# Kernel tuning notes

Measured on AMD Instinct MI355X. Metric: run time of the kernel, lower is better.

Reference implementation:

```python
import jax, jax.numpy as jnp
import numpy as np

B, S, E, H = 2, 2048, 1024, 16
HD = E // H
DFF = 4 * E
LN_EPS = 1e-5


def _layernorm(x, g, b):
    mu = jnp.mean(x, axis=-1, keepdims=True)
    var = jnp.mean(jnp.square(x - mu), axis=-1, keepdims=True)
    return (x - mu) * jax.lax.rsqrt(var + LN_EPS) * g + b


def setup_inputs() -> dict:
    key = jax.random.key(0)
    ks = jax.random.split(key, 6)
    inp = {
        "x": jax.random.normal(ks[0], (B, S, E), jnp.float32),
        "ln1_g": jnp.ones((E,), jnp.float32),
        "ln1_b": jnp.zeros((E,), jnp.float32),
        "ln2_g": jnp.ones((E,), jnp.float32),
        "ln2_b": jnp.zeros((E,), jnp.float32),
        # OptimizedPoincareBallLinear init: randn * 0.1, zero bias
        "w_qkv": jax.random.normal(ks[1], (3 * E, E), jnp.float32) * 0.1,
        "b_qkv": jnp.zeros((3 * E,), jnp.float32),
        "w_ao": jax.random.normal(ks[2], (E, E), jnp.float32) * 0.1,
        "b_ao": jnp.zeros((E,), jnp.float32),
        "w_fc": jax.random.normal(ks[3], (DFF, E), jnp.float32) * 0.1,
        "b_fc": jnp.zeros((DFF,), jnp.float32),
        "w_po": jax.random.normal(ks[4], (E, DFF), jnp.float32) * 0.1,
        "b_po": jnp.zeros((E,), jnp.float32),
    }
    return inp


def reference(x, ln1_g, ln1_b, ln2_g, ln2_b, w_qkv, b_qkv, w_ao, b_ao,
              w_fc, b_fc, w_po, b_po):
    # --- attention branch ---
    h = _layernorm(x, ln1_g, ln1_b)
    qkv = h @ w_qkv.T + b_qkv                       # [B,S,3E]
    qkv = qkv.reshape(B, S, H, 3 * HD).transpose(0, 2, 1, 3)  # [B,H,S,3hd]
    q, k, v = jnp.split(qkv, 3, axis=-1)            # each [B,H,S,hd]
    scores = jnp.einsum('bhqd,bhkd->bhqk', q, k) / jnp.sqrt(
        jnp.asarray(HD, jnp.float32))
    causal = jnp.tril(jnp.ones((S, S), bool))        # attn_bias[:, :, :S, :S]
    scores = jnp.where(causal, scores, jnp.finfo(scores.dtype).min)
    attn_w = jax.nn.softmax(scores, axis=-1)         # dropout p=0.1 inactive (eval)
    attn = jnp.einsum('bhqk,bhkd->bhqd', attn_w, v)  # [B,H,S,hd]
    attn = attn.transpose(0, 2, 1, 3).reshape(B, S, E)
    attn = attn @ w_ao.T + b_ao
    x = x + attn
    # --- MLP branch ---
    h2 = _layernorm(x, ln2_g, ln2_b)
    h2 = h2 @ w_fc.T + b_fc
    h2 = jax.nn.gelu(h2, approximate=True)           # GPT-2 gelu_new
    h2 = h2 @ w_po.T + b_po
    x = x + h2
    return x
```

## Files before the change

kernel.cpp:

```cpp
#include <hip/hip_runtime.h>
#include <cstddef>
#include <cstdint>

#define Bc 2
#define Sc 2048
#define Ec 1024
#define Hc 16
#define HDc 64
#define DFFc 4096
#define ROWS (Bc * Sc)

typedef _Float16 half8v __attribute__((ext_vector_type(8)));
typedef _Float16 half4v __attribute__((ext_vector_type(4)));
typedef float f32x4 __attribute__((ext_vector_type(4)));
typedef _Float16 h16;

__device__ inline void gld_lds16(const void* g, void* l) {
    __builtin_amdgcn_global_load_lds(
        (const __attribute__((address_space(1))) void*)g,
        (__attribute__((address_space(3))) void*)l, 16, 0, 0);
}

__device__ inline float gelu_new(float x) {
    float x2 = x * x;
    float u = x * fmaf(0.07135481627362f, x2, 1.5957691216057308f);
    return x / (1.0f + __expf(-u));
}

__global__ __launch_bounds__(256) void cvt4_kernel(
    const float* __restrict__ a,
    const float* __restrict__ b,
    const float* __restrict__ c,
    const float* __restrict__ d,
    h16* __restrict__ out)
{
    int bid = blockIdx.x;
    const float* src;
    size_t obase;
    int base;
    if (bid < 3072)      { src = a; obase = 0;       base = bid; }
    else if (bid < 4096) { src = b; obase = 3145728; base = bid - 3072; }
    else if (bid < 8192) { src = c; obase = 4194304; base = bid - 4096; }
    else                 { src = d; obase = 8388608; base = bid - 8192; }
    int i = base * 1024 + threadIdx.x * 4;
    float4 v = *(const float4*)(src + i);
    half4v o;
    o.x = (h16)v.x; o.y = (h16)v.y; o.z = (h16)v.z; o.w = (h16)v.w;
    *(half4v*)(out + obase + i) = o;
}

__device__ inline float block_sum256(float v, float* sb) {
    #pragma unroll
    for (int o = 32; o > 0; o >>= 1) v += __shfl_down(v, o, 64);
    int lane = threadIdx.x & 63, w = threadIdx.x >> 6;
    if (lane == 0) sb[w] = v;
    __syncthreads();
    float r = sb[0] + sb[1] + sb[2] + sb[3];
    __syncthreads();
    return r;
}

__global__ __launch_bounds__(256) void ln_kernel(const float* __restrict__ x,
                                                 const float* __restrict__ g,
                                                 const float* __restrict__ b,
                                                 h16* __restrict__ out) {
    __shared__ float sb[4];
    int row = blockIdx.x;
    int t = threadIdx.x;
    const float* xr = x + (size_t)row * Ec;
    float4 v = ((const float4*)xr)[t];
    float s = v.x + v.y + v.z + v.w;
    float mu = block_sum256(s, sb) * (1.0f / Ec);
    float dx = v.x - mu, dy = v.y - mu, dz = v.z - mu, dw = v.w - mu;
    float ss = dx * dx + dy * dy + dz * dz + dw * dw;
    float var = block_sum256(ss, sb) * (1.0f / Ec);
    float inv = rsqrtf(var + 1e-5f);
    float4 gv = ((const float4*)g)[t];
    float4 bv = ((const float4*)b)[t];
    half4v o;
    o.x = (h16)(dx * inv * gv.x + bv.x);
    o.y = (h16)(dy * inv * gv.y + bv.y);
    o.z = (h16)(dz * inv * gv.z + bv.z);
    o.w = (h16)(dw * inv * gv.w + bv.w);
    ((half4v*)(out + (size_t)row * Ec))[t] = o;
}

template <int EPI, typename OutT>
__global__ __launch_bounds__(256) void gemm_mfma(
    const h16* __restrict__ A, const h16* __restrict__ W,
    const float* __restrict__ bias, const float* __restrict__ R,
    OutT* __restrict__ C, int M, int N, int K)
{
    __shared__ h16 As[2][128 * 32];
    __shared__ h16 Ws[2][128 * 32];

    const int t = threadIdx.x;
    const int lane = t & 63, wv = t >> 6;
    const int wm = wv >> 1, wn = wv & 1;
    const int c15 = lane & 15, q = lane >> 4;
    const int row0 = blockIdx.y * 128, col0 = blockIdx.x * 128;
    const int arow = t >> 2, acol = (t & 3) << 3;

    const h16* ap0 = A + (size_t)(row0 + arow) * K + acol;
    const h16* ap1 = ap0 + (size_t)64 * K;
    const h16* wp0 = W + (size_t)(col0 + arow) * K + acol;
    const h16* wp1 = wp0 + (size_t)64 * K;
    h16* lA0[2]; h16* lA1[2]; h16* lW0[2]; h16* lW1[2];
    #pragma unroll
    for (int kk = 0; kk < 2; ++kk) {
        lA0[kk] = &As[kk][arow * 32 + acol];
        lA1[kk] = &As[kk][(64 + arow) * 32 + acol];
        lW0[kk] = &Ws[kk][arow * 32 + acol];
        lW1[kk] = &Ws[kk][(64 + arow) * 32 + acol];
    }

    f32x4 acc[4][4];
    #pragma unroll
    for (int i = 0; i < 4; ++i)
        #pragma unroll
        for (int j = 0; j < 4; ++j)
            acc[i][j] = (f32x4){0.f, 0.f, 0.f, 0.f};

    for (int k0 = 0; k0 < K; k0 += 64) {
        __syncthreads();
        #pragma unroll
        for (int kk = 0; kk < 2; ++kk) {
            gld_lds16(ap0 + kk * 32, lA0[kk]);
            gld_lds16(ap1 + kk * 32, lA1[kk]);
            gld_lds16(wp0 + kk * 32, lW0[kk]);
            gld_lds16(wp1 + kk * 32, lW1[kk]);
        }
        __syncthreads();

        #pragma unroll
        for (int kk = 0; kk < 2; ++kk) {
            half8v af[4], bf[4];
            #pragma unroll
            for (int i = 0; i < 4; ++i)
                af[i] = *(const half8v*)&As[kk][(wm * 64 + i * 16 + c15) * 32 + q * 8];
            #pragma unroll
            for (int j = 0; j < 4; ++j)
                bf[j] = *(const half8v*)&Ws[kk][(wn * 64 + j * 16 + c15) * 32 + q * 8];
            #pragma unroll
            for (int i = 0; i < 4; ++i)
                #pragma unroll
                for (int j = 0; j < 4; ++j)
                    acc[i][j] = __builtin_amdgcn_mfma_f32_16x16x32_f16(af[i], bf[j], acc[i][j], 0, 0, 0);
        }
        ap0 += 64; ap1 += 64; wp0 += 64; wp1 += 64;
    }

    #pragma unroll
    for (int i = 0; i < 4; ++i) {
        #pragma unroll
        for (int j = 0; j < 4; ++j) {
            int col = col0 + wn * 64 + j * 16 + c15;
            float bv = bias[col];
            #pragma unroll
            for (int r = 0; r < 4; ++r) {
                int row = row0 + wm * 64 + i * 16 + q * 4 + r;
                size_t off = (size_t)row * N + col;
                float v = acc[i][j][r] + bv;
                if (EPI == 1) v += R[off];
                if (EPI == 2) v = gelu_new(v);
                if (sizeof(OutT) == 2) ((h16*)C)[off] = (h16)v;
                else ((float*)C)[off] = v;
            }
        }
    }
}

template <int EPI, typename OutT>
__global__ __launch_bounds__(256) void gemm_k64(
    const h16* __restrict__ A, const h16* __restrict__ W,
    const float* __restrict__ bias, const float* __restrict__ R,
    OutT* __restrict__ C, int M, int N, int K)
{
    __shared__ h16 As[4][64 * 32];
    __shared__ h16 Ws[4][128 * 32];

    const int t = threadIdx.x;
    const int lane = t & 63, wv = t >> 6;
    const int wm = wv >> 1, wn = wv & 1;
    const int c15 = lane & 15, q = lane >> 4;
    const int id = blockIdx.x;
    const int cx = id & 7;
    const int kq = id >> 3;
    const int bx = kq & 7;
    const int by = ((kq >> 3) << 3) | cx;
    const int row0 = by * 64, col0 = bx * 128;
    const int arow = t >> 2, acol = (t & 3) << 3;

    const h16* ap  = A + (size_t)(row0 + arow) * K + acol;
    const h16* wp0 = W + (size_t)(col0 + arow) * K + acol;
    const h16* wp1 = wp0 + (size_t)64 * K;
    h16* lA[4]; h16* lW0[4]; h16* lW1[4];
    #pragma unroll
    for (int kk = 0; kk < 4; ++kk) {
        lA[kk]  = &As[kk][arow * 32 + acol];
        lW0[kk] = &Ws[kk][arow * 32 + acol];
        lW1[kk] = &Ws[kk][(64 + arow) * 32 + acol];
    }

    f32x4 acc[2][4];
    #pragma unroll
    for (int i = 0; i < 2; ++i)
        #pragma unroll
        for (int j = 0; j < 4; ++j)
            acc[i][j] = (f32x4){0.f, 0.f, 0.f, 0.f};

    for (int k0 = 0; k0 < K; k0 += 128) {
        __syncthreads();
        #pragma unroll
        for (int kk = 0; kk < 4; ++kk) {
            gld_lds16(ap  + kk * 32, lA[kk]);
            gld_lds16(wp0 + kk * 32, lW0[kk]);
            gld_lds16(wp1 + kk * 32, lW1[kk]);
        }
        __syncthreads();

        #pragma unroll
        for (int kk = 0; kk < 4; ++kk) {
            half8v af[2], bf[4];
            #pragma unroll
            for (int i = 0; i < 2; ++i)
                af[i] = *(const half8v*)&As[kk][(wm * 32 + i * 16 + c15) * 32 + q * 8];
            #pragma unroll
            for (int j = 0; j < 4; ++j)
                bf[j] = *(const half8v*)&Ws[kk][(wn * 64 + j * 16 + c15) * 32 + q * 8];
            #pragma unroll
            for (int i = 0; i < 2; ++i)
                #pragma unroll
                for (int j = 0; j < 4; ++j)
                    acc[i][j] = __builtin_amdgcn_mfma_f32_16x16x32_f16(af[i], bf[j], acc[i][j], 0, 0, 0);
        }
        ap += 128; wp0 += 128; wp1 += 128;
    }

    #pragma unroll
    for (int i = 0; i < 2; ++i) {
        #pragma unroll
        for (int j = 0; j < 4; ++j) {
            int col = col0 + wn * 64 + j * 16 + c15;
            float bv = bias[col];
            #pragma unroll
            for (int r = 0; r < 4; ++r) {
                int row = row0 + wm * 32 + i * 16 + q * 4 + r;
                size_t off = (size_t)row * N + col;
                float v = acc[i][j][r] + bv;
                if (EPI == 1) v += R[off];
                if (EPI == 2) v = gelu_new(v);
                if (sizeof(OutT) == 2) ((h16*)C)[off] = (h16)v;
                else ((float*)C)[off] = v;
            }
        }
    }
}

__global__ __launch_bounds__(256, 4) void attn_mfma(const h16* __restrict__ qkv,
                                                    h16* __restrict__ attn) {
    __shared__ h16 Ks[2][2][64 * 32];
    __shared__ h16 Vt[2][64 * 32];
    __shared__ h16 Ps[4][16 * 72];

    const int t = threadIdx.x;
    const int lane = t & 63, wv = t >> 6;
    const int c15 = lane & 15, q = lane >> 4;
    const int bh = blockIdx.x, b = bh >> 4, h = bh & 15;
    const int ja = 31 - blockIdx.y;
    const int qbase = ja * 64 + wv * 16;
    const int SE = 3 * Ec;
    const size_t hbase = (size_t)b * Sc * SE + (size_t)h * (3 * HDc);

    half8v qf[2];
    #pragma unroll
    for (int kk = 0; kk < 2; ++kk) {
        qf[kk] = *(const half8v*)(qkv + hbase + (size_t)(qbase + c15) * SE + kk * 32 + q * 8);
        qf[kk] *= (h16)0.125f;
    }

    f32x4 O[4];
    #pragma unroll
    for (int n = 0; n < 4; ++n) O[n] = (f32x4){0.f, 0.f, 0.f, 0.f};
    float mi = -3e38f, li = 0.f;

    const int krow = t >> 2, kcol = (t & 3) << 3;
    const int vkey = t & 31, vd0 = (t >> 5) << 3;
    half8v vreg[2];

    auto stageK = [&](int kt, int bf) {
        #pragma unroll
        for (int p = 0; p < 2; ++p)
            gld_lds16(qkv + hbase + (size_t)(kt * 64 + krow) * SE + HDc + p * 32 + kcol,
                      &Ks[bf][p][krow * 32 + kcol]);
    };
    auto loadV = [&](int kt) {
        #pragma unroll
        for (int p = 0; p < 2; ++p)
            vreg[p] = *(const half8v*)(qkv + hbase +
                        (size_t)(kt * 64 + p * 32 + vkey) * SE + 2 * HDc + vd0);
    };
    auto scatV = [&]() {
        #pragma unroll
        for (int p = 0; p < 2; ++p)
            #pragma unroll
            for (int u = 0; u < 8; ++u)
                Vt[p][(vd0 + u) * 32 + vkey] = vreg[p][u];
    };

    stageK(0, 0);
    loadV(0);
    scatV();
    __syncthreads();

    for (int kt = 0; kt <= ja; ++kt) {
        const int bf = kt & 1;
        if (kt < ja) { stageK(kt + 1, bf ^ 1); loadV(kt + 1); }

        f32x4 st[4];
        #pragma unroll
        for (int j = 0; j < 4; ++j) {
            half8v kf0 = *(const half8v*)&Ks[bf][0][(j * 16 + c15) * 32 + q * 8];
            half8v kf1 = *(const half8v*)&Ks[bf][1][(j * 16 + c15) * 32 + q * 8];
            f32x4 z = (f32x4){0.f, 0.f, 0.f, 0.f};
            z = __builtin_amdgcn_mfma_f32_16x16x32_f16(kf0, qf[0], z, 0, 0, 0);
            st[j] = __builtin_amdgcn_mfma_f32_16x16x32_f16(kf1, qf[1], z, 0, 0, 0);
        }

        if (kt == ja) {
            const int rowloc = wv * 16 + c15;
            #pragma unroll
            for (int j = 0; j < 4; ++j)
                #pragma unroll
                for (int r = 0; r < 4; ++r)
                    if (j * 16 + q * 4 + r > rowloc) st[j][r] = -3e38f;
        }

        float mx = mi;
        #pragma unroll
        for (int j = 0; j < 4; ++j)
            #pragma unroll
            for (int r = 0; r < 4; ++r) mx = fmaxf(mx, st[j][r]);
        mx = fmaxf(mx, __shfl_xor(mx, 16, 64));
        mx = fmaxf(mx, __shfl_xor(mx, 32, 64));
        float al = __expf(mi - mx);
        mi = mx;
        float ps = 0.f;
        #pragma unroll
        for (int j = 0; j < 4; ++j) {
            half4v pk;
            #pragma unroll
            for (int r = 0; r < 4; ++r) {
                float p = __expf(st[j][r] - mx);
                ps += p;
                pk[r] = (h16)p;
            }
            *(half4v*)&Ps[wv][c15 * 72 + j * 16 + q * 4] = pk;
        }
        ps += __shfl_xor(ps, 16, 64);
        ps += __shfl_xor(ps, 32, 64);
        li = li * al + ps;

        half8v pb0 = *(const half8v*)&Ps[wv][c15 * 72 + q * 8];
        half8v pb1 = *(const half8v*)&Ps[wv][c15 * 72 + 32 + q * 8];
        #pragma unroll
        for (int n = 0; n < 4; ++n) {
            #pragma unroll
            for (int r = 0; r < 4; ++r) O[n][r] *= al;
            half8v va0 = *(const half8v*)&Vt[0][(n * 16 + c15) * 32 + q * 8];
            half8v va1 = *(const half8v*)&Vt[1][(n * 16 + c15) * 32 + q * 8];
            O[n] = __builtin_amdgcn_mfma_f32_16x16x32_f16(va0, pb0, O[n], 0, 0, 0);
            O[n] = __builtin_amdgcn_mfma_f32_16x16x32_f16(va1, pb1, O[n], 0, 0, 0);
        }

        if (kt < ja) {
            __syncthreads();
            scatV();
            __syncthreads();
        }
    }

    float rl = 1.0f / li;
    #pragma unroll
    for (int n = 0; n < 4; ++n) {
        half4v o4;
        #pragma unroll
        for (int r = 0; r < 4; ++r) o4[r] = (h16)(O[n][r] * rl);
        *(half4v*)(attn + ((size_t)(b * Sc + qbase + c15)) * Ec + h * HDc + n * 16 + q * 4) = o4;
    }
}

extern "C" void kernel_launch(void* const* d_in, const int* in_sizes, int n_in,
                              void* d_out, int out_size, void* d_ws, size_t ws_size,
                              hipStream_t stream) {
    const float* x     = (const float*)d_in[0];
    const float* ln1_g = (const float*)d_in[1];
    const float* ln1_b = (const float*)d_in[2];
    const float* ln2_g = (const float*)d_in[3];
    const float* ln2_b = (const float*)d_in[4];
    const float* w_qkv = (const float*)d_in[5];
    const float* b_qkv = (const float*)d_in[6];
    const float* w_ao  = (const float*)d_in[7];
    const float* b_ao  = (const float*)d_in[8];
    const float* w_fc  = (const float*)d_in[9];
    const float* b_fc  = (const float*)d_in[10];
    const float* w_po  = (const float*)d_in[11];
    const float* b_po  = (const float*)d_in[12];
    float* out = (float*)d_out;

    char* w = (char*)d_ws;
    h16* wqkv = (h16*)(w);
    h16* wao  = (h16*)(w + 6291456);
    h16* wfc  = (h16*)(w + 8388608);
    h16* wpo  = (h16*)(w + 16777216);
    h16* hb   = (h16*)(w + 25165824);
    h16* qkv  = (h16*)(w + 33554432);
    h16* attn = (h16*)(w + 58720256);
    float* x1 = (float*)(w + 67108864);
    h16* ff   = qkv;

    dim3 blk(256);

    cvt4_kernel<<<dim3(12288), blk, 0, stream>>>(w_qkv, w_ao, w_fc, w_po, wqkv);

    ln_kernel<<<dim3(ROWS), blk, 0, stream>>>(x, ln1_g, ln1_b, hb);
    gemm_mfma<0, h16><<<dim3(3 * Ec / 128, ROWS / 128), blk, 0, stream>>>(
        hb, wqkv, b_qkv, nullptr, qkv, ROWS, 3 * Ec, Ec);
    attn_mfma<<<dim3(Bc * Hc, 32), blk, 0, stream>>>(qkv, attn);
    gemm_k64<1, float><<<dim3(512), blk, 0, stream>>>(
        attn, wao, b_ao, x, x1, ROWS, Ec, Ec);
    ln_kernel<<<dim3(ROWS), blk, 0, stream>>>(x1, ln2_g, ln2_b, hb);
    gemm_mfma<2, h16><<<dim3(DFFc / 128, ROWS / 128), blk, 0, stream>>>(
        hb, wfc, b_fc, nullptr, ff, ROWS, DFFc, Ec);
    gemm_k64<1, float><<<dim3(512), blk, 0, stream>>>(
        ff, wpo, b_po, x1, out, ROWS, Ec, DFFc);
}
```

Baseline: 343.3 us.

## Double-buffer LDS staging in GEMM kernels to overlap loads with MFMA

Both GEMM kernels now use ping-pong LDS buffers. The next K-slice's global-to-LDS loads are issued before computing on the current slice, with one barrier per half-step. Before, each iteration loaded the whole K tile, waited, then computed, so memory latency was exposed. The risk is that barrier waits on the async LDS loads still serialise, and the per-stage K chunk is now smaller.

```diff
diff --git a/kernel.cpp b/kernel.cpp
--- a/kernel.cpp
+++ b/kernel.cpp
@@ -105,14 +105,6 @@
     const h16* ap1 = ap0 + (size_t)64 * K;
     const h16* wp0 = W + (size_t)(col0 + arow) * K + acol;
     const h16* wp1 = wp0 + (size_t)64 * K;
-    h16* lA0[2]; h16* lA1[2]; h16* lW0[2]; h16* lW1[2];
-    #pragma unroll
-    for (int kk = 0; kk < 2; ++kk) {
-        lA0[kk] = &As[kk][arow * 32 + acol];
-        lA1[kk] = &As[kk][(64 + arow) * 32 + acol];
-        lW0[kk] = &Ws[kk][arow * 32 + acol];
-        lW1[kk] = &Ws[kk][(64 + arow) * 32 + acol];
-    }
 
     f32x4 acc[4][4];
     #pragma unroll
@@ -121,34 +113,43 @@
         for (int j = 0; j < 4; ++j)
             acc[i][j] = (f32x4){0.f, 0.f, 0.f, 0.f};
 
-    for (int k0 = 0; k0 < K; k0 += 64) {
+    auto stageL = [&](h16* asB, h16* wsB, int koff) {
+        gld_lds16(ap0 + koff, asB + arow * 32 + acol);
+        gld_lds16(ap1 + koff, asB + (64 + arow) * 32 + acol);
+        gld_lds16(wp0 + koff, wsB + arow * 32 + acol);
+        gld_lds16(wp1 + koff, wsB + (64 + arow) * 32 + acol);
+    };
+    auto computeL = [&](const h16* asB, const h16* wsB) {
+        half8v af[4], bfv[4];
+        #pragma unroll
+        for (int i = 0; i < 4; ++i)
+            af[i] = *(const half8v*)&asB[(wm * 64 + i * 16 + c15) * 32 + q * 8];
+        #pragma unroll
+        for (int j = 0; j < 4; ++j)
+            bfv[j] = *(const half8v*)&wsB[(wn * 64 + j * 16 + c15) * 32 + q * 8];
+        #pragma unroll
+        for (int i = 0; i < 4; ++i)
+            #pragma unroll
+            for (int j = 0; j < 4; ++j)
+                acc[i][j] = __builtin_amdgcn_mfma_f32_16x16x32_f16(af[i], bfv[j], acc[i][j], 0, 0, 0);
+    };
+
+    stageL(As[0], Ws[0], 0);
+    __syncthreads();
+
+    int k0 = 0;
+    for (; k0 < K - 64; k0 += 64) {
+        stageL(As[1], Ws[1], k0 + 32);
+        computeL(As[0], Ws[0]);
         __syncthreads();
-        #pragma unroll
-        for (int kk = 0; kk < 2; ++kk) {
-            gld_lds16(ap0 + kk * 32, lA0[kk]);
-            gld_lds16(ap1 + kk * 32, lA1[kk]);
-            gld_lds16(wp0 + kk * 32, lW0[kk]);
-            gld_lds16(wp1 + kk * 32, lW1[kk]);
-        }
+        stageL(As[0], Ws[0], k0 + 64);
+        computeL(As[1], Ws[1]);
         __syncthreads();
-
-        #pragma unroll
-        for (int kk = 0; kk < 2; ++kk) {
-            half8v af[4], bf[4];
-            #pragma unroll
-            for (int i = 0; i < 4; ++i)
-                af[i] = *(const half8v*)&As[kk][(wm * 64 + i * 16 + c15) * 32 + q * 8];
-            #pragma unroll
-            for (int j = 0; j < 4; ++j)
-                bf[j] = *(const half8v*)&Ws[kk][(wn * 64 + j * 16 + c15) * 32 + q * 8];
-            #pragma unroll
-            for (int i = 0; i < 4; ++i)
-                #pragma unroll
-                for (int j = 0; j < 4; ++j)
-                    acc[i][j] = __builtin_amdgcn_mfma_f32_16x16x32_f16(af[i], bf[j], acc[i][j], 0, 0, 0);
-        }
-        ap0 += 64; ap1 += 64; wp0 += 64; wp1 += 64;
-    }
+    }
+    stageL(As[1], Ws[1], k0 + 32);
+    computeL(As[0], Ws[0]);
+    __syncthreads();
+    computeL(As[1], Ws[1]);
 
     #pragma unroll
     for (int i = 0; i < 4; ++i) {
@@ -176,8 +177,8 @@
     const float* __restrict__ bias, const float* __restrict__ R,
     OutT* __restrict__ C, int M, int N, int K)
 {
-    __shared__ h16 As[4][64 * 32];
-    __shared__ h16 Ws[4][128 * 32];
+    __shared__ h16 As[2][2][64 * 32];
+    __shared__ h16 Ws[2][2][128 * 32];
 
     const int t = threadIdx.x;
     const int lane = t & 63, wv = t >> 6;
@@ -194,13 +195,6 @@
     const h16* ap  = A + (size_t)(row0 + arow) * K + acol;
     const h16* wp0 = W + (size_t)(col0 + arow) * K + acol;
     const h16* wp1 = wp0 + (size_t)64 * K;
-    h16* lA[4]; h16* lW0[4]; h16* lW1[4];
-    #pragma unroll
-    for (int kk = 0; kk < 4; ++kk) {
-        lA[kk]  = &As[kk][arow * 32 + acol];
-        lW0[kk] = &Ws[kk][arow * 32 + acol];
-        lW1[kk] = &Ws[kk][(64 + arow) * 32 + acol];
-    }
 
     f32x4 acc[2][4];
     #pragma unroll
@@ -209,33 +203,48 @@
         for (int j = 0; j < 4; ++j)
             acc[i][j] = (f32x4){0.f, 0.f, 0.f, 0.f};
 
-    for (int k0 = 0; k0 < K; k0 += 128) {
-        __syncthreads();
-        #pragma unroll
-        for (int kk = 0; kk < 4; ++kk) {
-            gld_lds16(ap  + kk * 32, lA[kk]);
-            gld_lds16(wp0 + kk * 32, lW0[kk]);
-            gld_lds16(wp1 + kk * 32, lW1[kk]);
-        }
-        __syncthreads();
-
-        #pragma unroll
-        for (int kk = 0; kk < 4; ++kk) {
-            half8v af[2], bf[4];
+    auto stageL = [&](h16 (*asB)[64 * 32], h16 (*wsB)[128 * 32], int koff) {
+        #pragma unroll
+        for (int kk = 0; kk < 2; ++kk) {
+            gld_lds16(ap  + koff + kk * 32, &asB[kk][arow * 32 + acol]);
+            gld_lds16(wp0 + koff + kk * 32, &wsB[kk][arow * 32 + acol]);
+            gld_lds16(wp1 + koff + kk * 32, &wsB[kk][(64 + arow) * 32 + acol]);
+        }
+    };
+    auto computeL = [&](const h16 (*asB)[64 * 32], const h16 (*wsB)[128 * 32]) {
+        #pragma unroll
+        for (int kk = 0; kk < 2; ++kk) {
+            half8v af[2], bfv[4];
             #pragma unroll
             for (int i = 0; i < 2; ++i)
-                af[i] = *(const half8v*)&As[kk][(wm * 32 + i * 16 + c15) * 32 + q * 8];
+                af[i] = *(const half8v*)&asB[kk][(wm * 32 + i * 16 + c15) * 32 + q * 8];
             #pragma unroll
             for (int j = 0; j < 4; ++j)
-                bf[j] = *(const half8v*)&Ws[kk][(wn * 64 + j * 16 + c15) * 32 + q * 8];
+                bfv[j] = *(const half8v*)&wsB[kk][(wn * 64 + j * 16 + c15) * 32 + q * 8];
             #pragma unroll
             for (int i = 0; i < 2; ++i)
                 #pragma unroll
                 for (int j = 0; j < 4; ++j)
-                    acc[i][j] = __builtin_amdgcn_mfma_f32_16x16x32_f16(af[i], bf[j], acc[i][j], 0, 0, 0);
-        }
-        ap += 128; wp0 += 128; wp1 += 128;
-    }
+                    acc[i][j] = __builtin_amdgcn_mfma_f32_16x16x32_f16(af[i], bfv[j], acc[i][j], 0, 0, 0);
+        }
+    };
+
+    stageL(As[0], Ws[0], 0);
+    __syncthreads();
+
+    int k0 = 0;
+    for (; k0 < K - 128; k0 += 128) {
+        stageL(As[1], Ws[1], k0 + 64);
+        computeL(As[0], Ws[0]);
+        __syncthreads();
+        stageL(As[0], Ws[0], k0 + 128);
+        computeL(As[1], Ws[1]);
+        __syncthreads();
+    }
+    stageL(As[1], Ws[1], k0 + 64);
+    computeL(As[0], Ws[0]);
+    __syncthreads();
+    computeL(As[1], Ws[1]);
 
     #pragma unroll
     for (int i = 0; i < 2; ++i) {
```

Measured after the change: 351.9 us. +2.5%, slower.
